# Performance work log

Measured on AMD Instinct MI355X. Metric: run time of the kernel, lower is better.

The kernel has to match this reference:

```python
import jax, jax.numpy as jnp
from jax import lax
import numpy as np

OBS_DIM, PROJ, HID, LAT = 128, 64, 256, 24
B, T = 1024, 256


def setup_inputs() -> dict:
    key = jax.random.key(0)
    ks = jax.random.split(key, 10)
    obs = jax.random.normal(ks[0], (B, T, OBS_DIM), dtype=jnp.float32)
    is_init = jax.random.randint(ks[1], (B, T, 1), 0, 2) > 0
    hx = jnp.zeros((B, HID), dtype=jnp.float32)
    # params (fan-in scaled)
    W_in = jax.random.normal(ks[2], (OBS_DIM, PROJ), dtype=jnp.float32) / np.sqrt(OBS_DIM)
    b_in = jnp.zeros((PROJ,), dtype=jnp.float32)
    W_ih = jax.random.normal(ks[3], (PROJ, 3 * HID), dtype=jnp.float32) / np.sqrt(PROJ)
    b_ih = jnp.zeros((3 * HID,), dtype=jnp.float32)
    W_hh = jax.random.normal(ks[4], (HID, 3 * HID), dtype=jnp.float32) / np.sqrt(HID)
    b_hh = jnp.zeros((3 * HID,), dtype=jnp.float32)
    W_out = jax.random.normal(ks[5], (HID, LAT), dtype=jnp.float32) / np.sqrt(HID)
    b_out = jnp.zeros((LAT,), dtype=jnp.float32)
    return dict(obs=obs, is_init=is_init, hx=hx, W_in=W_in, b_in=b_in,
                W_ih=W_ih, b_ih=b_ih, W_hh=W_hh, b_hh=b_hh,
                W_out=W_out, b_out=b_out)


def reference(obs, is_init, hx, W_in, b_in, W_ih, b_ih, W_hh, b_hh, W_out, b_out):
    # input projection: [B,T,OBS] -> [B,T,64]
    x = obs @ W_in + b_in
    # precompute input-side gates once: [B,T,3H]
    gx = jnp.swapaxes(x @ W_ih + b_ih, 0, 1)           # [T,B,3H]
    mask = jnp.swapaxes(is_init.astype(hx.dtype), 0, 1)  # [T,B,1]

    def step(h, inp):
        g, m = inp
        h = h * (1.0 - m)                # episode-reset masking
        gh = h @ W_hh + b_hh             # [B,3H]
        gxr, gxz, gxn = jnp.split(g, 3, axis=-1)
        ghr, ghz, ghn = jnp.split(gh, 3, axis=-1)
        r = jax.nn.sigmoid(gxr + ghr)
        z = jax.nn.sigmoid(gxz + ghz)
        n = jnp.tanh(gxn + r * ghn)
        h_new = (1.0 - z) * n + z * h
        return h_new, h_new

    h_final, ys = lax.scan(step, hx, (gx, mask))
    seq = jnp.swapaxes(ys, 0, 1)         # [B,T,H]
    mish = seq * jnp.tanh(jax.nn.softplus(seq))
    out = mish @ W_out + b_out           # [B,T,LAT]
    return out, h_final
```

## Files before the change

### kernel.cpp

```cpp
#include <hip/hip_runtime.h>
#include <cstdint>
#include <cstddef>

#define OBS_DIMM 128
#define PROJJ    64
#define HIDD     256
#define LATT     24
#define BBATCH   1024
#define TTIME    256
#define NGATE    768
#define MBLK     16
#define CHUNK    64
#define NGROUP   64
#define NCHUNK   4
#define HSTR     264

using bf16x8 = __attribute__((ext_vector_type(8))) short;
using f32x4  = __attribute__((ext_vector_type(4))) float;

static __device__ __forceinline__ unsigned short f2bf(float f) {
    unsigned u = __builtin_bit_cast(unsigned, f);
    u += 0x7fffu + ((u >> 16) & 1u);
    return (unsigned short)(u >> 16);
}
static __device__ __forceinline__ float bf2f(unsigned short h) {
    return __builtin_bit_cast(float, ((unsigned)h) << 16);
}
static __device__ __forceinline__ unsigned cvt_pk_bf16(float lo, float hi) {
    unsigned r;
    asm("v_cvt_pk_bf16_f32 %0, %1, %2" : "=v"(r) : "v"(lo), "v"(hi));
    return r;
}
static __device__ __forceinline__ float fexp2(float x) { return __builtin_amdgcn_exp2f(x); }
static __device__ __forceinline__ float frcp (float x) { return __builtin_amdgcn_rcpf(x); }
static __device__ __forceinline__ float sigmoid_(float x) { return frcp(1.f + fexp2(-1.44269504f * x)); }
static __device__ __forceinline__ float tanh_(float x)    { return 1.f - 2.f * frcp(fexp2(2.88539008f * x) + 1.f); }
static __device__ __forceinline__ float mish_f(float x) {
    float ex = fexp2(1.44269504f * x);
    float t1 = 1.f + ex;
    return x * (1.f - 2.f * frcp(t1 * t1 + 1.f));
}

static __device__ __forceinline__ void bar_lgkm() {
    asm volatile("s_waitcnt lgkmcnt(0)\n\ts_barrier" ::: "memory");
}

#define MFMA16(a, b, c) __builtin_amdgcn_mfma_f32_16x16x32_bf16((a), (b), (c), 0, 0, 0)

__global__ void prep_kernel(const float* __restrict__ W_in, const float* __restrict__ b_in,
                            const float* __restrict__ W_ih, const float* __restrict__ b_ih,
                            const float* __restrict__ W_hh, const float* __restrict__ W_out,
                            unsigned short* __restrict__ wsWhh, unsigned short* __restrict__ wsWih,
                            unsigned short* __restrict__ wsWin, unsigned short* __restrict__ wsWo,
                            float* __restrict__ wsBx) {
    int idx = blockIdx.x * 256 + threadIdx.x;
    if (idx < 196608) {
        int f = idx >> 9, rem = idx & 511, l = rem >> 3, jj = rem & 7;
        int q = l >> 4, c16 = l & 15;
        int g = f % 3, f2 = f / 3, i = f2 & 1, f3 = f2 >> 1;
        int kt = f3 & 7, w = f3 >> 3;
        int s5 = q * 8 + jj;
        int k = kt * 32 + ((s5 & 1) << 4) + (s5 >> 1);
        int n = g * 256 + (2 * w + i) * 16 + c16;
        wsWhh[idx] = f2bf(W_hh[k * NGATE + n]);
    } else if (idx < 245760) {
        int d = idx - 196608;
        int f = d >> 9, rem = d & 511, l = rem >> 3, jj = rem & 7;
        int q = l >> 4, c16 = l & 15;
        int g = f % 3, f2 = f / 3, i = f2 & 1, f3 = f2 >> 1;
        int kt = f3 & 1, w = f3 >> 1;
        int k = kt * 32 + q * 8 + jj;
        int n = g * 256 + (2 * w + i) * 16 + c16;
        wsWih[d] = f2bf(W_ih[k * NGATE + n]);
    } else if (idx < 253952) {
        int d = idx - 245760;
        int f = d >> 9, rem = d & 511, l = rem >> 3, jj = rem & 7;
        int q = l >> 4, nl = l & 15;
        int nt = f & 3, kt = f >> 2;
        int k = kt * 32 + q * 8 + jj;
        int n = nt * 16 + nl;
        wsWin[d] = f2bf(W_in[k * PROJJ + n]);
    } else if (idx < 262144) {
        int d = idx - 253952;
        int f = d >> 9, rem = d & 511, l = rem >> 3, jj = rem & 7;
        int q = l >> 4, nl = l & 15;
        int kt = f & 7, nt = f >> 3;
        int s5 = q * 8 + jj;
        int k = kt * 32 + ((s5 & 1) << 4) + (s5 >> 1);
        int n = nt * 16 + nl;
        wsWo[d] = f2bf((n < LATT) ? W_out[k * LATT + n] : 0.f);
    } else if (idx < 262912) {
        int n = idx - 262144;
        float s = b_ih[n];
        for (int j = 0; j < PROJJ; ++j) s += b_in[j] * W_ih[j * NGATE + n];
        wsBx[n] = s;
    }
}

__global__ __launch_bounds__(256)
void xproj_kernel(const float* __restrict__ obs, const unsigned short* __restrict__ wsWin,
                  unsigned short* __restrict__ xf) {
    __shared__ __align__(16) unsigned short ldsO[8 * 16 * 136];
    __shared__ __align__(16) unsigned short sWin[8192];
    __shared__ __align__(16) unsigned short sXP[4][1040];
    const int tid = threadIdx.x, w = tid >> 6, lane = tid & 63, q = lane >> 4, c16 = lane & 15;
    const int bid = blockIdx.x;
    const int g = bid >> 5, tc = bid & 31;
    const int t0x = tc * 8, b0x = g * 16;

    {
        const uint4* s = (const uint4*)wsWin; uint4* d = (uint4*)sWin;
#pragma unroll
        for (int r = 0; r < 4; ++r) d[r * 256 + tid] = s[r * 256 + tid];
    }
    {
        const int tl = tid >> 5, f4 = tid & 31;
        const float* base = obs + ((size_t)b0x * TTIME + t0x + tl) * OBS_DIMM + f4 * 4;
#pragma unroll
        for (int p = 0; p < 16; ++p) {
            float4 v = *(const float4*)(base + (size_t)p * TTIME * OBS_DIMM);
            unsigned lo = cvt_pk_bf16(v.x, v.y);
            unsigned hi = cvt_pk_bf16(v.z, v.w);
            *(uint2*)(ldsO + (tl * 16 + p) * 136 + f4 * 4) = make_uint2(lo, hi);
        }
    }
    __syncthreads();

    for (int s = 0; s < 2; ++s) {
        const int tl = w * 2 + s;
        f32x4 acc[4];
#pragma unroll
        for (int nt = 0; nt < 4; ++nt) acc[nt] = (f32x4){0.f, 0.f, 0.f, 0.f};
#pragma unroll
        for (int kt = 0; kt < 4; ++kt) {
            bf16x8 a = *(const bf16x8*)(ldsO + (tl * 16 + c16) * 136 + kt * 32 + q * 8);
#pragma unroll
            for (int nt = 0; nt < 4; ++nt)
                acc[nt] = MFMA16(a, *(const bf16x8*)(sWin + (kt * 4 + nt) * 512 + lane * 8), acc[nt]);
        }
#pragma unroll
        for (int nt = 0; nt < 4; ++nt) {
            int unit = nt * 16 + c16;
            int ktp = unit >> 5, qp = (unit >> 3) & 3, jjp = unit & 7;
#pragma unroll
            for (int r = 0; r < 4; ++r)
                sXP[w][(qp * 16 + q * 4 + r) * 16 + ktp * 8 + jjp] = f2bf(acc[nt][r]);
        }
        unsigned short* dst = xf + (size_t)(g * 256 + t0x + tl) * 1024 + lane * 16;
        *(bf16x8*)dst       = *(const bf16x8*)(sXP[w] + lane * 16);
        *(bf16x8*)(dst + 8) = *(const bf16x8*)(sXP[w] + lane * 16 + 8);
    }
}

__global__ __launch_bounds__(512, 2)
void gru_kernel(const int* __restrict__ is_init, const float* __restrict__ hx,
                const float* __restrict__ b_hh, const float* __restrict__ b_out,
                const unsigned short* __restrict__ wsWhh, const unsigned short* __restrict__ wsWih,
                const unsigned short* __restrict__ wsWo, const float* __restrict__ wsBx,
                const unsigned short* __restrict__ xf,
                float* __restrict__ out, float* __restrict__ hfin) {
    __shared__ __align__(16) unsigned short sWih[49152];
    __shared__ __align__(16) unsigned short sWo[8192];
    __shared__ __align__(16) unsigned short sH[2][MBLK * HSTR];
    __shared__ __align__(16) unsigned short sM[3][MBLK * HSTR];
    __shared__ __align__(16) float sBias[1056];
    __shared__ unsigned sInit[MBLK][8];
    __shared__ int sT;

    const int tid  = threadIdx.x;
    const int w    = tid >> 6;
    const int lane = tid & 63;
    const int q    = lane >> 4;
    const int c16  = lane & 15;
    const int bid  = blockIdx.x;
    const int g    = bid & (NGROUP - 1);
    const int ch   = bid >> 6;
    const int b0   = g * MBLK;
    const int t0   = ch * CHUNK;
    const int tend = t0 + CHUNK;

    const unsigned short* whh_p = wsWhh + (size_t)w * 24576 + lane * 8;
    bf16x8 Whh[48];
#pragma unroll
    for (int f = 0; f < 48; ++f)
        Whh[f] = *(const bf16x8*)(whh_p + (size_t)f * 512);

    {
        const uint4* s1 = (const uint4*)wsWih; uint4* d1 = (uint4*)sWih;
#pragma unroll
        for (int r = 0; r < 12; ++r) d1[r * 512 + tid] = s1[r * 512 + tid];
        const uint4* s3 = (const uint4*)wsWo;  uint4* d3 = (uint4*)sWo;
#pragma unroll
        for (int r = 0; r < 2; ++r) d3[r * 512 + tid] = s3[r * 512 + tid];
    }
    if (tid < 256) {
        sBias[tid]       = wsBx[tid] + b_hh[tid];
        sBias[256 + tid] = wsBx[HIDD + tid] + b_hh[HIDD + tid];
        sBias[512 + tid] = wsBx[2 * HIDD + tid];
        sBias[768 + tid] = b_hh[2 * HIDD + tid];
    } else if (tid < 288) {
        int col = tid - 256;
        sBias[1024 + col] = (col < LATT) ? b_out[col] : 0.f;
    }
    if (tid < 128) {
        int b = tid >> 3, wd = tid & 7;
        unsigned m = 0;
        const int* ip = is_init + (size_t)(b0 + b) * TTIME + wd * 32;
#pragma unroll
        for (int j = 0; j < 32; ++j) m |= (ip[j] != 0 ? 1u : 0u) << j;
        sInit[b][wd] = m;
    }
    if (tid == 0) sT = (ch == 0) ? 0 : 0x7fffffff;
    __syncthreads();

    if (ch > 0 && tid < MBLK) {
        int fs = 0;
        for (int wi = (t0 >> 5) - 1; wi >= 0; --wi) {
            unsigned m = sInit[tid][wi];
            if (wi == 0) m &= ~1u;
            if (m) { fs = wi * 32 + 31 - __builtin_clz(m); break; }
        }
        atomicMin(&sT, fs);
    }
    __syncthreads();
    const int tstart = sT;

    unsigned hReg[4];
#pragma unroll
    for (int r = 0; r < 4; ++r) {
        int b = q * 4 + r;
        unsigned rbit = (sInit[b][tstart >> 5] >> (tstart & 31)) & 1u;
        float h0v = 0.f, h1v = 0.f;
        if (tstart == 0 && !rbit) {
            const float* hp = hx + (size_t)(b0 + b) * HIDD;
            h0v = hp[2 * w * 16 + c16];
            h1v = hp[(2 * w + 1) * 16 + c16];
        }
        unsigned pk = (unsigned)f2bf(h0v) | ((unsigned)f2bf(h1v) << 16);
        hReg[r] = pk;
        ((unsigned*)sH[0])[b * 132 + w * 16 + c16] = pk;
    }
    bf16x8 X0, X1;
    {
        const unsigned short* xp = xf + (size_t)(g * 256 + tstart) * 1024 + lane * 16;
        X0 = *(const bf16x8*)xp; X1 = *(const bf16x8*)(xp + 8);
    }
    const unsigned short* wihp = sWih + w * 6144 + lane * 8;
    unsigned short* sHr = sH[0];
    unsigned short* sHw = sH[1];
    unsigned short* pWm = sM[tstart % 3];
    unsigned short* pR1 = sM[(tstart + 2) % 3];
    unsigned short* pR2 = sM[(tstart + 1) % 3];
    __syncthreads();

    f32x4 accR[2], accZ[2], accXN[2], accHN[2];
    auto accfill = [&]() {
#pragma unroll
        for (int i = 0; i < 2; ++i) {
            int u = (2 * w + i) * 16 + c16;
            float vR = sBias[u], vZ = sBias[256 + u], vX = sBias[512 + u], vH = sBias[768 + u];
            accR[i]  = (f32x4){vR, vR, vR, vR};
            accZ[i]  = (f32x4){vZ, vZ, vZ, vZ};
            accXN[i] = (f32x4){vX, vX, vX, vX};
            accHN[i] = (f32x4){vH, vH, vH, vH};
            accR[i]  = MFMA16(X0, *(const bf16x8*)(wihp + (i * 3 + 0) * 512), accR[i]);
            accZ[i]  = MFMA16(X0, *(const bf16x8*)(wihp + (i * 3 + 1) * 512), accZ[i]);
            accXN[i] = MFMA16(X0, *(const bf16x8*)(wihp + (i * 3 + 2) * 512), accXN[i]);
            accR[i]  = MFMA16(X1, *(const bf16x8*)(wihp + (6 + i * 3 + 0) * 512), accR[i]);
            accZ[i]  = MFMA16(X1, *(const bf16x8*)(wihp + (6 + i * 3 + 1) * 512), accZ[i]);
            accXN[i] = MFMA16(X1, *(const bf16x8*)(wihp + (6 + i * 3 + 2) * 512), accXN[i]);
        }
    };
    accfill();

    for (int t = tstart; t < tend; ++t) {
        {
            int tn = (t + 1 < TTIME) ? t + 1 : TTIME - 1;
            const unsigned short* xp = xf + (size_t)(g * 256 + tn) * 1024 + lane * 16;
            X0 = *(const bf16x8*)xp; X1 = *(const bf16x8*)(xp + 8);
        }
#pragma unroll
        for (int kt = 0; kt < 8; ++kt) {
            bf16x8 a = *(const bf16x8*)(sHr + c16 * HSTR + kt * 32 + q * 8);
#pragma unroll
            for (int i = 0; i < 2; ++i) {
                accR[i]  = MFMA16(a, Whh[kt * 6 + i * 3 + 0], accR[i]);
                accZ[i]  = MFMA16(a, Whh[kt * 6 + i * 3 + 1], accZ[i]);
                accHN[i] = MFMA16(a, Whh[kt * 6 + i * 3 + 2], accHN[i]);
            }
        }
        f32x4 oa;
        const bool doO = (t >= t0 + 2) && ((w >> 1) == (t & 3));
        if (doO) {
            int nt = w & 1;
            float bo = sBias[1024 + nt * 16 + c16];
            oa = (f32x4){bo, bo, bo, bo};
            const unsigned short* smp = pR2 + c16 * HSTR + q * 8;
#pragma unroll
            for (int kt = 0; kt < 8; ++kt)
                oa = MFMA16(*(const bf16x8*)(smp + kt * 32),
                            *(const bf16x8*)(sWo + (nt * 8 + kt) * 512 + lane * 8), oa);
        }
        int m4 = 0;
        if (t + 1 < tend) {
            int wd = (t + 1) >> 5, bt = (t + 1) & 31;
#pragma unroll
            for (int r = 0; r < 4; ++r)
                m4 |= (int)((sInit[q * 4 + r][wd] >> bt) & 1u) << r;
        }
        const bool emit = (t >= t0);
#pragma unroll
        for (int r = 0; r < 4; ++r) {
            int bl = q * 4 + r;
            float hs0 = bf2f((unsigned short)(hReg[r] & 0xffffu));
            float hs1 = bf2f((unsigned short)(hReg[r] >> 16));
            float rr0 = sigmoid_(accR[0][r]), rr1 = sigmoid_(accR[1][r]);
            float zz0 = sigmoid_(accZ[0][r]), zz1 = sigmoid_(accZ[1][r]);
            float nn0 = tanh_(accXN[0][r] + rr0 * accHN[0][r]);
            float nn1 = tanh_(accXN[1][r] + rr1 * accHN[1][r]);
            float h0 = (1.f - zz0) * nn0 + zz0 * hs0;
            float h1 = (1.f - zz1) * nn1 + zz1 * hs1;
            if (emit)
                ((unsigned*)pWm)[bl * 132 + w * 16 + c16] =
                    cvt_pk_bf16(mish_f(h0), mish_f(h1));
            if ((m4 >> r) & 1) { h0 = 0.f; h1 = 0.f; }
            unsigned pk = cvt_pk_bf16(h0, h1);
            hReg[r] = pk;
            ((unsigned*)sHw)[bl * 132 + w * 16 + c16] = pk;
        }
        if (doO) {
            int nt = w & 1, col = nt * 16 + c16, tb = t - 2;
            if (col < LATT) {
#pragma unroll
                for (int r = 0; r < 4; ++r)
                    out[((size_t)(b0 + q * 4 + r) * TTIME + tb) * LATT + col] = oa[r];
            }
        }
        if (t + 1 < tend) accfill();
        bar_lgkm();
        { unsigned short* tp = sHr; sHr = sHw; sHw = tp; }
        { unsigned short* tp = pWm; pWm = pR2; pR2 = pR1; pR1 = tp; }
    }

    if (w < 4) {
        int nt = w & 1;
        unsigned short* pR = (w < 2) ? pR2 : pR1;
        int tb = (w < 2) ? tend - 2 : tend - 1;
        float bo = sBias[1024 + nt * 16 + c16];
        f32x4 oa2 = (f32x4){bo, bo, bo, bo};
        const unsigned short* smp = pR + c16 * HSTR + q * 8;
#pragma unroll
        for (int kt = 0; kt < 8; ++kt)
            oa2 = MFMA16(*(const bf16x8*)(smp + kt * 32),
                         *(const bf16x8*)(sWo + (nt * 8 + kt) * 512 + lane * 8), oa2);
        int col = nt * 16 + c16;
        if (col < LATT) {
#pragma unroll
            for (int r = 0; r < 4; ++r)
                out[((size_t)(b0 + q * 4 + r) * TTIME + tb) * LATT + col] = oa2[r];
        }
    }
    if (ch == NCHUNK - 1) {
#pragma unroll
        for (int r = 0; r < 4; ++r) {
            float* hp = hfin + (size_t)(b0 + q * 4 + r) * HIDD;
            hp[2 * w * 16 + c16]       = bf2f((unsigned short)(hReg[r] & 0xffffu));
            hp[(2 * w + 1) * 16 + c16] = bf2f((unsigned short)(hReg[r] >> 16));
        }
    }
}

extern "C" void kernel_launch(void* const* d_in, const int* in_sizes, int n_in,
                              void* d_out, int out_size, void* d_ws, size_t ws_size,
                              hipStream_t stream) {
    const float* obs    = (const float*)d_in[0];
    const int*   isini  = (const int*)d_in[1];
    const float* hx     = (const float*)d_in[2];
    const float* W_in   = (const float*)d_in[3];
    const float* b_in   = (const float*)d_in[4];
    const float* W_ih   = (const float*)d_in[5];
    const float* b_ih   = (const float*)d_in[6];
    const float* W_hh   = (const float*)d_in[7];
    const float* b_hh   = (const float*)d_in[8];
    const float* W_out  = (const float*)d_in[9];
    const float* b_out  = (const float*)d_in[10];

    unsigned short* xfbuf = (unsigned short*)d_ws;
    unsigned short* wsWhh = xfbuf + (size_t)BBATCH * TTIME * 64;
    unsigned short* wsWih = wsWhh + 196608;
    unsigned short* wsWin = wsWih + 49152;
    unsigned short* wsWo  = wsWin + 8192;
    float*          wsBx  = (float*)(wsWo + 8192);

    float* outp = (float*)d_out;
    float* hfin = outp + (size_t)BBATCH * TTIME * LATT;

    prep_kernel<<<1027, 256, 0, stream>>>(W_in, b_in, W_ih, b_ih, W_hh, W_out,
                                          wsWhh, wsWih, wsWin, wsWo, wsBx);
    xproj_kernel<<<2048, 256, 0, stream>>>(obs, wsWin, xfbuf);
    gru_kernel<<<256, 512, 0, stream>>>(isini, hx, b_hh, b_out,
                                        wsWhh, wsWih, wsWo, wsBx, xfbuf, outp, hfin);
}
```

Baseline: 478.9 us.

## Regroup GRU blocks into 32-row batches with 1024 threads and shorter time chunks

Each GRU block now handles 32 batch rows with 16 waves, and each wave covers half the gate columns for both 16-row halves, so every W_hh fragment in registers is reused across two MFMA row tiles. W_ih fragments move from LDS into registers, and the reset mask is stored per timestep as a 32-bit batch mask. Time chunks shrink to 32 steps over 8 chunks, which shortens the serial chain per block. In exchange, the warm-up replay from the last reset can cover up to 224 extra steps in later chunks. The block now holds 1024 threads at one block per CU, and hidden-state LDS stores become 16-bit scattered writes.

New measurement: 788.5 us. 1.65x slower.

```diff
diff --git a/kernel.cpp b/kernel.cpp
--- a/kernel.cpp
+++ b/kernel.cpp
@@ -9,10 +9,10 @@
 #define BBATCH   1024
 #define TTIME    256
 #define NGATE    768
-#define MBLK     16
-#define CHUNK    64
-#define NGROUP   64
-#define NCHUNK   4
+#define MBLK     32
+#define CHUNK    32
+#define NGROUP   32
+#define NCHUNK   8
 #define HSTR     264
 
 using bf16x8 = __attribute__((ext_vector_type(8))) short;
@@ -152,100 +152,101 @@
     }
 }
 
-__global__ __launch_bounds__(512, 2)
+__global__ __launch_bounds__(1024, 1)
 void gru_kernel(const int* __restrict__ is_init, const float* __restrict__ hx,
                 const float* __restrict__ b_hh, const float* __restrict__ b_out,
                 const unsigned short* __restrict__ wsWhh, const unsigned short* __restrict__ wsWih,
                 const unsigned short* __restrict__ wsWo, const float* __restrict__ wsBx,
                 const unsigned short* __restrict__ xf,
                 float* __restrict__ out, float* __restrict__ hfin) {
-    __shared__ __align__(16) unsigned short sWih[49152];
     __shared__ __align__(16) unsigned short sWo[8192];
     __shared__ __align__(16) unsigned short sH[2][MBLK * HSTR];
     __shared__ __align__(16) unsigned short sM[3][MBLK * HSTR];
     __shared__ __align__(16) float sBias[1056];
-    __shared__ unsigned sInit[MBLK][8];
+    __shared__ unsigned sRstT[TTIME];
     __shared__ int sT;
 
     const int tid  = threadIdx.x;
-    const int w    = tid >> 6;
+    const int w16  = tid >> 6;
+    const int w8   = w16 >> 1;
+    const int ih   = w16 & 1;
     const int lane = tid & 63;
     const int q    = lane >> 4;
     const int c16  = lane & 15;
     const int bid  = blockIdx.x;
-    const int g    = bid & (NGROUP - 1);
-    const int ch   = bid >> 6;
-    const int b0   = g * MBLK;
+    const int gg   = bid & (NGROUP - 1);
+    const int ch   = bid >> 5;
+    const int b0   = gg * MBLK;
     const int t0   = ch * CHUNK;
     const int tend = t0 + CHUNK;
-
-    const unsigned short* whh_p = wsWhh + (size_t)w * 24576 + lane * 8;
-    bf16x8 Whh[48];
-#pragma unroll
-    for (int f = 0; f < 48; ++f)
-        Whh[f] = *(const bf16x8*)(whh_p + (size_t)f * 512);
-
-    {
-        const uint4* s1 = (const uint4*)wsWih; uint4* d1 = (uint4*)sWih;
-#pragma unroll
-        for (int r = 0; r < 12; ++r) d1[r * 512 + tid] = s1[r * 512 + tid];
-        const uint4* s3 = (const uint4*)wsWo;  uint4* d3 = (uint4*)sWo;
-#pragma unroll
-        for (int r = 0; r < 2; ++r) d3[r * 512 + tid] = s3[r * 512 + tid];
-    }
+    const int pcol = 32 * w8 + 2 * c16 + ih;
+
+    bf16x8 Whh[24];
+#pragma unroll
+    for (int kt = 0; kt < 8; ++kt)
+#pragma unroll
+        for (int gte = 0; gte < 3; ++gte)
+            Whh[kt * 3 + gte] = *(const bf16x8*)(wsWhh +
+                (size_t)(((w8 * 8 + kt) * 6 + ih * 3 + gte)) * 512 + lane * 8);
+    bf16x8 Wih[6];
+#pragma unroll
+    for (int kt = 0; kt < 2; ++kt)
+#pragma unroll
+        for (int gte = 0; gte < 3; ++gte)
+            Wih[kt * 3 + gte] = *(const bf16x8*)(wsWih +
+                (size_t)(((w8 * 2 + kt) * 6 + ih * 3 + gte)) * 512 + lane * 8);
+
+    ((uint4*)sWo)[tid] = ((const uint4*)wsWo)[tid];
     if (tid < 256) {
         sBias[tid]       = wsBx[tid] + b_hh[tid];
         sBias[256 + tid] = wsBx[HIDD + tid] + b_hh[HIDD + tid];
         sBias[512 + tid] = wsBx[2 * HIDD + tid];
         sBias[768 + tid] = b_hh[2 * HIDD + tid];
+        unsigned mbits = 0;
+#pragma unroll 4
+        for (int b = 0; b < MBLK; ++b)
+            mbits |= (is_init[(size_t)(b0 + b) * TTIME + tid] != 0 ? 1u : 0u) << b;
+        sRstT[tid] = mbits;
     } else if (tid < 288) {
         int col = tid - 256;
         sBias[1024 + col] = (col < LATT) ? b_out[col] : 0.f;
     }
-    if (tid < 128) {
-        int b = tid >> 3, wd = tid & 7;
-        unsigned m = 0;
-        const int* ip = is_init + (size_t)(b0 + b) * TTIME + wd * 32;
-#pragma unroll
-        for (int j = 0; j < 32; ++j) m |= (ip[j] != 0 ? 1u : 0u) << j;
-        sInit[b][wd] = m;
-    }
     if (tid == 0) sT = (ch == 0) ? 0 : 0x7fffffff;
     __syncthreads();
 
     if (ch > 0 && tid < MBLK) {
         int fs = 0;
-        for (int wi = (t0 >> 5) - 1; wi >= 0; --wi) {
-            unsigned m = sInit[tid][wi];
-            if (wi == 0) m &= ~1u;
-            if (m) { fs = wi * 32 + 31 - __builtin_clz(m); break; }
-        }
+        for (int tt = t0 - 1; tt > 0; --tt)
+            if ((sRstT[tt] >> tid) & 1u) { fs = tt; break; }
         atomicMin(&sT, fs);
     }
     __syncthreads();
     const int tstart = sT;
 
-    unsigned hReg[4];
-#pragma unroll
-    for (int r = 0; r < 4; ++r) {
-        int b = q * 4 + r;
-        unsigned rbit = (sInit[b][tstart >> 5] >> (tstart & 31)) & 1u;
-        float h0v = 0.f, h1v = 0.f;
-        if (tstart == 0 && !rbit) {
-            const float* hp = hx + (size_t)(b0 + b) * HIDD;
-            h0v = hp[2 * w * 16 + c16];
-            h1v = hp[(2 * w + 1) * 16 + c16];
-        }
-        unsigned pk = (unsigned)f2bf(h0v) | ((unsigned)f2bf(h1v) << 16);
-        hReg[r] = pk;
-        ((unsigned*)sH[0])[b * 132 + w * 16 + c16] = pk;
-    }
-    bf16x8 X0, X1;
+    const int u = (2 * w8 + ih) * 16 + c16;
+    unsigned hPk[4];
     {
-        const unsigned short* xp = xf + (size_t)(g * 256 + tstart) * 1024 + lane * 16;
-        X0 = *(const bf16x8*)xp; X1 = *(const bf16x8*)(xp + 8);
-    }
-    const unsigned short* wihp = sWih + w * 6144 + lane * 8;
+        unsigned rw0 = sRstT[tstart];
+#pragma unroll
+        for (int r = 0; r < 4; ++r) {
+            int bl0 = q * 4 + r, bl1 = 16 + q * 4 + r;
+            float h0v = 0.f, h1v = 0.f;
+            if (tstart == 0) {
+                if (!((rw0 >> bl0) & 1u)) h0v = hx[(size_t)(b0 + bl0) * HIDD + u];
+                if (!((rw0 >> bl1) & 1u)) h1v = hx[(size_t)(b0 + bl1) * HIDD + u];
+            }
+            unsigned pk = cvt_pk_bf16(h0v, h1v);
+            hPk[r] = pk;
+            sH[0][bl0 * HSTR + pcol] = (unsigned short)(pk & 0xffffu);
+            sH[0][bl1 * HSTR + pcol] = (unsigned short)(pk >> 16);
+        }
+    }
+    bf16x8 XA[2], XB[2];
+#pragma unroll
+    for (int m = 0; m < 2; ++m) {
+        const unsigned short* xp = xf + (size_t)((2 * gg + m) * 256 + tstart) * 1024 + lane * 16;
+        XA[m] = *(const bf16x8*)xp; XB[m] = *(const bf16x8*)(xp + 8);
+    }
     unsigned short* sHr = sH[0];
     unsigned short* sHw = sH[1];
     unsigned short* pWm = sM[tstart % 3];
@@ -253,22 +254,21 @@
     unsigned short* pR2 = sM[(tstart + 1) % 3];
     __syncthreads();
 
-    f32x4 accR[2], accZ[2], accXN[2], accHN[2];
+    f32x4 aR[2], aZ[2], aXN[2], aHN[2];
     auto accfill = [&]() {
-#pragma unroll
-        for (int i = 0; i < 2; ++i) {
-            int u = (2 * w + i) * 16 + c16;
-            float vR = sBias[u], vZ = sBias[256 + u], vX = sBias[512 + u], vH = sBias[768 + u];
-            accR[i]  = (f32x4){vR, vR, vR, vR};
-            accZ[i]  = (f32x4){vZ, vZ, vZ, vZ};
-            accXN[i] = (f32x4){vX, vX, vX, vX};
-            accHN[i] = (f32x4){vH, vH, vH, vH};
-            accR[i]  = MFMA16(X0, *(const bf16x8*)(wihp + (i * 3 + 0) * 512), accR[i]);
-            accZ[i]  = MFMA16(X0, *(const bf16x8*)(wihp + (i * 3 + 1) * 512), accZ[i]);
-            accXN[i] = MFMA16(X0, *(const bf16x8*)(wihp + (i * 3 + 2) * 512), accXN[i]);
-            accR[i]  = MFMA16(X1, *(const bf16x8*)(wihp + (6 + i * 3 + 0) * 512), accR[i]);
-            accZ[i]  = MFMA16(X1, *(const bf16x8*)(wihp + (6 + i * 3 + 1) * 512), accZ[i]);
-            accXN[i] = MFMA16(X1, *(const bf16x8*)(wihp + (6 + i * 3 + 2) * 512), accXN[i]);
+        float vR = sBias[u], vZ = sBias[256 + u], vX = sBias[512 + u], vH = sBias[768 + u];
+#pragma unroll
+        for (int m = 0; m < 2; ++m) {
+            aR[m]  = (f32x4){vR, vR, vR, vR};
+            aZ[m]  = (f32x4){vZ, vZ, vZ, vZ};
+            aXN[m] = (f32x4){vX, vX, vX, vX};
+            aHN[m] = (f32x4){vH, vH, vH, vH};
+            aR[m]  = MFMA16(XA[m], Wih[0], aR[m]);
+            aZ[m]  = MFMA16(XA[m], Wih[1], aZ[m]);
+            aXN[m] = MFMA16(XA[m], Wih[2], aXN[m]);
+            aR[m]  = MFMA16(XB[m], Wih[3], aR[m]);
+            aZ[m]  = MFMA16(XB[m], Wih[4], aZ[m]);
+            aXN[m] = MFMA16(XB[m], Wih[5], aXN[m]);
         }
     };
     accfill();
@@ -276,64 +276,66 @@
     for (int t = tstart; t < tend; ++t) {
         {
             int tn = (t + 1 < TTIME) ? t + 1 : TTIME - 1;
-            const unsigned short* xp = xf + (size_t)(g * 256 + tn) * 1024 + lane * 16;
-            X0 = *(const bf16x8*)xp; X1 = *(const bf16x8*)(xp + 8);
+#pragma unroll
+            for (int m = 0; m < 2; ++m) {
+                const unsigned short* xp = xf + (size_t)((2 * gg + m) * 256 + tn) * 1024 + lane * 16;
+                XA[m] = *(const bf16x8*)xp; XB[m] = *(const bf16x8*)(xp + 8);
+            }
         }
 #pragma unroll
         for (int kt = 0; kt < 8; ++kt) {
-            bf16x8 a = *(const bf16x8*)(sHr + c16 * HSTR + kt * 32 + q * 8);
-#pragma unroll
-            for (int i = 0; i < 2; ++i) {
-                accR[i]  = MFMA16(a, Whh[kt * 6 + i * 3 + 0], accR[i]);
-                accZ[i]  = MFMA16(a, Whh[kt * 6 + i * 3 + 1], accZ[i]);
-                accHN[i] = MFMA16(a, Whh[kt * 6 + i * 3 + 2], accHN[i]);
-            }
+            bf16x8 a0 = *(const bf16x8*)(sHr + c16 * HSTR + kt * 32 + q * 8);
+            bf16x8 a1 = *(const bf16x8*)(sHr + (16 + c16) * HSTR + kt * 32 + q * 8);
+            aR[0]  = MFMA16(a0, Whh[kt * 3 + 0], aR[0]);
+            aZ[0]  = MFMA16(a0, Whh[kt * 3 + 1], aZ[0]);
+            aHN[0] = MFMA16(a0, Whh[kt * 3 + 2], aHN[0]);
+            aR[1]  = MFMA16(a1, Whh[kt * 3 + 0], aR[1]);
+            aZ[1]  = MFMA16(a1, Whh[kt * 3 + 1], aZ[1]);
+            aHN[1] = MFMA16(a1, Whh[kt * 3 + 2], aHN[1]);
         }
         f32x4 oa;
-        const bool doO = (t >= t0 + 2) && ((w >> 1) == (t & 3));
+        const bool doO = (t >= t0 + 2) && ((w16 >> 2) == (t & 3));
+        int om = (w16 >> 1) & 1, ont = w16 & 1;
         if (doO) {
-            int nt = w & 1;
-            float bo = sBias[1024 + nt * 16 + c16];
+            float bo = sBias[1024 + ont * 16 + c16];
             oa = (f32x4){bo, bo, bo, bo};
-            const unsigned short* smp = pR2 + c16 * HSTR + q * 8;
+            const unsigned short* smp = pR2 + (om * 16 + c16) * HSTR + q * 8;
 #pragma unroll
             for (int kt = 0; kt < 8; ++kt)
                 oa = MFMA16(*(const bf16x8*)(smp + kt * 32),
-                            *(const bf16x8*)(sWo + (nt * 8 + kt) * 512 + lane * 8), oa);
-        }
-        int m4 = 0;
-        if (t + 1 < tend) {
-            int wd = (t + 1) >> 5, bt = (t + 1) & 31;
-#pragma unroll
-            for (int r = 0; r < 4; ++r)
-                m4 |= (int)((sInit[q * 4 + r][wd] >> bt) & 1u) << r;
-        }
+                            *(const bf16x8*)(sWo + (ont * 8 + kt) * 512 + lane * 8), oa);
+        }
+        unsigned rw = (t + 1 < tend) ? sRstT[t + 1] : 0u;
         const bool emit = (t >= t0);
 #pragma unroll
         for (int r = 0; r < 4; ++r) {
-            int bl = q * 4 + r;
-            float hs0 = bf2f((unsigned short)(hReg[r] & 0xffffu));
-            float hs1 = bf2f((unsigned short)(hReg[r] >> 16));
-            float rr0 = sigmoid_(accR[0][r]), rr1 = sigmoid_(accR[1][r]);
-            float zz0 = sigmoid_(accZ[0][r]), zz1 = sigmoid_(accZ[1][r]);
-            float nn0 = tanh_(accXN[0][r] + rr0 * accHN[0][r]);
-            float nn1 = tanh_(accXN[1][r] + rr1 * accHN[1][r]);
-            float h0 = (1.f - zz0) * nn0 + zz0 * hs0;
-            float h1 = (1.f - zz1) * nn1 + zz1 * hs1;
-            if (emit)
-                ((unsigned*)pWm)[bl * 132 + w * 16 + c16] =
-                    cvt_pk_bf16(mish_f(h0), mish_f(h1));
-            if ((m4 >> r) & 1) { h0 = 0.f; h1 = 0.f; }
-            unsigned pk = cvt_pk_bf16(h0, h1);
-            hReg[r] = pk;
-            ((unsigned*)sHw)[bl * 132 + w * 16 + c16] = pk;
+            int bl0 = q * 4 + r, bl1 = 16 + q * 4 + r;
+            float h0 = bf2f((unsigned short)(hPk[r] & 0xffffu));
+            float h1 = bf2f((unsigned short)(hPk[r] >> 16));
+            float rr0 = sigmoid_(aR[0][r]), rr1 = sigmoid_(aR[1][r]);
+            float zz0 = sigmoid_(aZ[0][r]), zz1 = sigmoid_(aZ[1][r]);
+            float nn0 = tanh_(aXN[0][r] + rr0 * aHN[0][r]);
+            float nn1 = tanh_(aXN[1][r] + rr1 * aHN[1][r]);
+            float hn0 = (1.f - zz0) * nn0 + zz0 * h0;
+            float hn1 = (1.f - zz1) * nn1 + zz1 * h1;
+            if (emit) {
+                unsigned mp = cvt_pk_bf16(mish_f(hn0), mish_f(hn1));
+                pWm[bl0 * HSTR + pcol] = (unsigned short)(mp & 0xffffu);
+                pWm[bl1 * HSTR + pcol] = (unsigned short)(mp >> 16);
+            }
+            if ((rw >> bl0) & 1u) hn0 = 0.f;
+            if ((rw >> bl1) & 1u) hn1 = 0.f;
+            unsigned pk = cvt_pk_bf16(hn0, hn1);
+            hPk[r] = pk;
+            sHw[bl0 * HSTR + pcol] = (unsigned short)(pk & 0xffffu);
+            sHw[bl1 * HSTR + pcol] = (unsigned short)(pk >> 16);
         }
         if (doO) {
-            int nt = w & 1, col = nt * 16 + c16, tb = t - 2;
+            int col = ont * 16 + c16, tb = t - 2;
             if (col < LATT) {
 #pragma unroll
                 for (int r = 0; r < 4; ++r)
-                    out[((size_t)(b0 + q * 4 + r) * TTIME + tb) * LATT + col] = oa[r];
+                    out[((size_t)(b0 + om * 16 + q * 4 + r) * TTIME + tb) * LATT + col] = oa[r];
             }
         }
         if (t + 1 < tend) accfill();
@@ -342,30 +344,29 @@
         { unsigned short* tp = pWm; pWm = pR2; pR2 = pR1; pR1 = tp; }
     }
 
-    if (w < 4) {
-        int nt = w & 1;
-        unsigned short* pR = (w < 2) ? pR2 : pR1;
-        int tb = (w < 2) ? tend - 2 : tend - 1;
-        float bo = sBias[1024 + nt * 16 + c16];
+    if (w16 < 8) {
+        int om = (w16 >> 1) & 1, ont = w16 & 1;
+        unsigned short* pR = (w16 < 4) ? pR2 : pR1;
+        int tb = (w16 < 4) ? tend - 2 : tend - 1;
+        float bo = sBias[1024 + ont * 16 + c16];
         f32x4 oa2 = (f32x4){bo, bo, bo, bo};
-        const unsigned short* smp = pR + c16 * HSTR + q * 8;
+        const unsigned short* smp = pR + (om * 16 + c16) * HSTR + q * 8;
 #pragma unroll
         for (int kt = 0; kt < 8; ++kt)
             oa2 = MFMA16(*(const bf16x8*)(smp + kt * 32),
-                         *(const bf16x8*)(sWo + (nt * 8 + kt) * 512 + lane * 8), oa2);
-        int col = nt * 16 + c16;
+                         *(const bf16x8*)(sWo + (ont * 8 + kt) * 512 + lane * 8), oa2);
+        int col = ont * 16 + c16;
         if (col < LATT) {
 #pragma unroll
             for (int r = 0; r < 4; ++r)
-                out[((size_t)(b0 + q * 4 + r) * TTIME + tb) * LATT + col] = oa2[r];
+                out[((size_t)(b0 + om * 16 + q * 4 + r) * TTIME + tb) * LATT + col] = oa2[r];
         }
     }
     if (ch == NCHUNK - 1) {
 #pragma unroll
         for (int r = 0; r < 4; ++r) {
-            float* hp = hfin + (size_t)(b0 + q * 4 + r) * HIDD;
-            hp[2 * w * 16 + c16]       = bf2f((unsigned short)(hReg[r] & 0xffffu));
-            hp[(2 * w + 1) * 16 + c16] = bf2f((unsigned short)(hReg[r] >> 16));
+            hfin[(size_t)(b0 + q * 4 + r) * HIDD + u]      = bf2f((unsigned short)(hPk[r] & 0xffffu));
+            hfin[(size_t)(b0 + 16 + q * 4 + r) * HIDD + u] = bf2f((unsigned short)(hPk[r] >> 16));
         }
     }
 }
@@ -398,6 +399,6 @@
     prep_kernel<<<1027, 256, 0, stream>>>(W_in, b_in, W_ih, b_ih, W_hh, W_out,
                                           wsWhh, wsWih, wsWin, wsWo, wsBx);
     xproj_kernel<<<2048, 256, 0, stream>>>(obs, wsWin, xfbuf);
-    gru_kernel<<<256, 512, 0, stream>>>(isini, hx, b_hh, b_out,
-                                        wsWhh, wsWih, wsWo, wsBx, xfbuf, outp, hfin);
-}
+    gru_kernel<<<256, 1024, 0, stream>>>(isini, hx, b_hh, b_out,
+                                         wsWhh, wsWih, wsWo, wsBx, xfbuf, outp, hfin);
+}
```
